# Performance work log

Hardware: AMD Instinct MI355X
Metric: run time of the kernel (lower is better)

Reference implementation:

```python
import jax, jax.numpy as jnp
import numpy as np

B, H, S, D = 8, 16, 1024, 64

def setup_inputs() -> dict:
    key = jax.random.key(0)
    kq, kk, kv, km = jax.random.split(key, 4)
    Q = jax.random.normal(kq, (B, H, S, D), dtype=jnp.float32)
    K = jax.random.normal(kk, (B, H, S, D), dtype=jnp.float32)
    V = jax.random.normal(kv, (B, H, S, D), dtype=jnp.float32)
    attn_mask = jax.random.randint(km, (B, H, S, S), 0, 2).astype(bool)
    return {"Q": Q, "K": K, "V": V, "attn_mask": attn_mask}

def reference(Q, K, V, attn_mask):
    # scores = Q @ K^T  (NOTE: source has no 1/sqrt(d) scaling)
    scores = jnp.einsum("bhqd,bhkd->bhqk", Q, K)
    # source uses masked_fill_(mask, 1e-9), i.e. masked positions become 1e-9 (not -inf)
    scores = jnp.where(attn_mask, jnp.float32(1e-9), scores)
    attn = jax.nn.softmax(scores, axis=-1)
    context = jnp.einsum("bhqk,bhkd->bhqd", attn, V)
    return context, attn
```

## Files before the change

### kernel.cpp

```cpp
#include <hip/hip_runtime.h>

#define Sn 1024
#define Dn 64
#define PH_LD 1032
#define K_LD 72
#define V_LD 72

typedef short v8s __attribute__((ext_vector_type(8)));
typedef unsigned short v8u __attribute__((ext_vector_type(8)));
typedef _Float16 v8h __attribute__((ext_vector_type(8)));
typedef float v4f __attribute__((ext_vector_type(4)));
typedef int   v4i __attribute__((ext_vector_type(4)));

#define LGKM0()  asm volatile("s_waitcnt lgkmcnt(0)" ::: "memory")
#define SBAR()   do { asm volatile("" ::: "memory"); __builtin_amdgcn_s_barrier(); \
                      __builtin_amdgcn_sched_barrier(0); } while (0)

__device__ __forceinline__ unsigned short f2bf(float x) {
    union { float f; unsigned u; } v; v.f = x;
    return (unsigned short)((v.u + 0x7FFFu + ((v.u >> 16) & 1u)) >> 16);
}
__device__ __forceinline__ float bf2f(unsigned short h) {
    union { float f; unsigned u; } v; v.u = ((unsigned)h) << 16;
    return v.f;
}
__device__ __forceinline__ void split2(float x, unsigned short& h, unsigned short& l) {
    unsigned short hs = f2bf(x);
    h = hs; l = f2bf(x - bf2f(hs));
}

__global__ __launch_bounds__(256) void prep_kh(const float* __restrict__ K,
    unsigned short* __restrict__ KF)
{
    const int bh = blockIdx.x >> 4, kt = blockIdx.x & 15;
    const int t = threadIdx.x;
    const int w = t >> 6, lane = t & 63;
    const int fr = lane & 15, g = lane >> 4;
    const float* src = K + (((size_t)(bh << 10) + (kt << 6) + (w << 4) + fr) << 6);
    const v4f a0 = __builtin_nontemporal_load((const v4f*)(src + (g << 3)));
    const v4f a1 = __builtin_nontemporal_load((const v4f*)(src + (g << 3) + 4));
    const v4f b0 = __builtin_nontemporal_load((const v4f*)(src + 32 + (g << 3)));
    const v4f b1 = __builtin_nontemporal_load((const v4f*)(src + 32 + (g << 3) + 4));
    v8h c0, c1;
    #pragma unroll
    for (int j = 0; j < 4; ++j) {
        c0[j] = (_Float16)a0[j]; c0[4 + j] = (_Float16)a1[j];
        c1[j] = (_Float16)b0[j]; c1[4 + j] = (_Float16)b1[j];
    }
    unsigned short* dst = KF + ((size_t)bh << 16) + ((size_t)((kt << 2) + w) << 10) + (lane << 3);
    *(v8h*)(dst)       = c0;
    *(v8h*)(dst + 512) = c1;
}

__global__ __launch_bounds__(256) void prep_vf(const float* __restrict__ V,
    unsigned short* __restrict__ VF)
{
    __shared__ float Ts[64][65];
    const int bh = blockIdx.x >> 4, kt = blockIdx.x & 15;
    const int t = threadIdx.x;
    {
        const int r = t >> 2, cs = (t & 3) << 4;
        const float* src = V + ((size_t)bh * Sn + (kt << 6) + r) * Dn + cs;
        const v4f a = __builtin_nontemporal_load((const v4f*)src);
        const v4f b = __builtin_nontemporal_load((const v4f*)src + 1);
        const v4f c = __builtin_nontemporal_load((const v4f*)src + 2);
        const v4f d = __builtin_nontemporal_load((const v4f*)src + 3);
        #pragma unroll
        for (int j = 0; j < 4; ++j) {
            Ts[r][cs + j]      = a[j];
            Ts[r][cs + 4 + j]  = b[j];
            Ts[r][cs + 8 + j]  = c[j];
            Ts[r][cs + 12 + j] = d[j];
        }
    }
    __syncthreads();
    {
        const int w = t >> 6, lane = t & 63;
        const int fr = lane & 15, g = lane >> 4;
        const int d = (w << 4) + fr;
        unsigned short* dst = VF + ((size_t)bh << 16) + ((size_t)((kt << 2) + w) << 10) + (lane << 3);
        v8u o0, o1;
        #pragma unroll
        for (int j = 0; j < 8; ++j) o0[j] = f2bf(Ts[(g << 3) + j][d]);
        #pragma unroll
        for (int j = 0; j < 8; ++j) o1[j] = f2bf(Ts[32 + (g << 3) + j][d]);
        *(v8u*)dst         = o0;
        *(v8u*)(dst + 512) = o1;
    }
}

__global__ __launch_bounds__(256) void prep_m(const int* __restrict__ M,
    unsigned long long* __restrict__ MW)
{
    const int NW = 2097152;
    const int lane = threadIdx.x & 63;
    const int wave = (blockIdx.x << 2) + (threadIdx.x >> 6);
    const int nwaves = gridDim.x << 2;
    for (int w0 = wave << 3; w0 < NW; w0 += nwaves << 3) {
        unsigned long long b[8];
        #pragma unroll
        for (int s = 0; s < 8; ++s) {
            const int v = __builtin_nontemporal_load(&M[((size_t)(w0 + s) << 6) + lane]);
            b[s] = __ballot(v != 0);
        }
        if (lane == 0) {
            ulonglong2* dst = (ulonglong2*)(MW + w0);
            ulonglong2 p0, p1, p2, p3;
            p0.x = b[0]; p0.y = b[1]; p1.x = b[2]; p1.y = b[3];
            p2.x = b[4]; p2.y = b[5]; p3.x = b[6]; p3.y = b[7];
            dst[0] = p0; dst[1] = p1; dst[2] = p2; dst[3] = p3;
        }
    }
}

__global__ __launch_bounds__(256, 4) void fused_attn_f(
    const unsigned short* __restrict__ KFG, const unsigned short* __restrict__ VFG,
    const float* __restrict__ Q, const unsigned long long* __restrict__ MW,
    float* __restrict__ attnO, float* __restrict__ ctxO)
{
    __shared__ unsigned short Ph[16][PH_LD];
    __shared__ float rsumW[4][16];
    __shared__ float invL[16];

    const int tid  = threadIdx.x;
    const int lane = tid & 63;
    const int w    = tid >> 6;
    const int fr   = lane & 15;
    const int g    = lane >> 4;

    const int swz = ((blockIdx.x & 7) << 10) + (blockIdx.x >> 3);
    const int bh = swz >> 6;
    const int q0 = (swz & 63) << 4;

    const float* Qb = Q + (size_t)bh * Sn * Dn + (size_t)q0 * Dn;
    float*       Ab = attnO + (size_t)bh * Sn * Sn + (size_t)q0 * Sn;
    float*       Cb = ctxO  + (size_t)bh * Sn * Dn + (size_t)q0 * Dn;
    const unsigned short* KFb = KFG + ((size_t)bh << 16);
    const unsigned short* VFb = VFG + ((size_t)bh << 16);
    const unsigned long long* mwp = MW + ((size_t)bh << 14) + ((size_t)(q0 + fr) << 4);

    v8h qf0, qf1;
    {
        const float* qp = Qb + fr * Dn + (g << 3);
        const v4f x0a = *(const v4f*)qp;
        const v4f x0b = *(const v4f*)(qp + 4);
        const v4f x1a = *(const v4f*)(qp + 32);
        const v4f x1b = *(const v4f*)(qp + 36);
        #pragma unroll
        for (int j = 0; j < 4; ++j) {
            qf0[j] = (_Float16)x0a[j]; qf0[4 + j] = (_Float16)x0b[j];
            qf1[j] = (_Float16)x1a[j]; qf1[4 + j] = (_Float16)x1b[j];
        }
    }

    const int sh = (w << 4) + (g << 2);

#define LDK(kt, k0_, k1_) do {                                                     \
        const unsigned short* _p = KFb + ((size_t)(((kt) << 2) + w) << 10) + (lane << 3); \
        k0_ = *(const v8h*)_p;  k1_ = *(const v8h*)(_p + 512);                     \
    } while (0)

#define STEPA(k0_, k1_, mwv, kt) do {                                              \
        v4f acc = {0.f, 0.f, 0.f, 0.f};                                            \
        __builtin_amdgcn_s_setprio(1);                                             \
        acc = __builtin_amdgcn_mfma_f32_16x16x32_f16(k0_, qf0, acc, 0, 0, 0);      \
        acc = __builtin_amdgcn_mfma_f32_16x16x32_f16(k1_, qf1, acc, 0, 0, 0);      \
        __builtin_amdgcn_s_setprio(0);                                             \
        const unsigned mb = (unsigned)((mwv) >> sh);                               \
        const float e0 = (mb & 1u) ? 1.0f : __expf(acc[0]);                        \
        const float e1 = (mb & 2u) ? 1.0f : __expf(acc[1]);                        \
        const float e2 = (mb & 4u) ? 1.0f : __expf(acc[2]);                        \
        const float e3 = (mb & 8u) ? 1.0f : __expf(acc[3]);                        \
        rs += (e0 + e1) + (e2 + e3);                                               \
        ushort4 pk;                                                                \
        pk.x = f2bf(e0); pk.y = f2bf(e1); pk.z = f2bf(e2); pk.w = f2bf(e3);        \
        *(ushort4*)&Ph[fr][((kt) << 6) + (w << 4) + (g << 2)] = pk;                \
    } while (0)

    float rs = 0.f;

    {
        v8h k0s[4], k1s[4];
        unsigned long long mk[4];
        LDK(0, k0s[0], k1s[0]);
        LDK(1, k0s[1], k1s[1]);
        LDK(2, k0s[2], k1s[2]);
        LDK(3, k0s[3], k1s[3]);
        mk[0] = mwp[0]; mk[1] = mwp[1]; mk[2] = mwp[2]; mk[3] = mwp[3];
        #pragma unroll
        for (int kt = 0; kt < 16; ++kt) {
            STEPA(k0s[kt & 3], k1s[kt & 3], mk[kt & 3], kt);
            if (kt + 4 < 16) {
                LDK(kt + 4, k0s[kt & 3], k1s[kt & 3]);
                mk[kt & 3] = mwp[kt + 4];
            }
        }
    }

    rs += __shfl_xor(rs, 16);
    rs += __shfl_xor(rs, 32);
    if (g == 0) rsumW[w][fr] = rs;
    __builtin_amdgcn_sched_barrier(0);
    LGKM0();
    SBAR();
    if (tid < 16) {
        const float s = rsumW[0][tid] + rsumW[1][tid] + rsumW[2][tid] + rsumW[3][tid];
        invL[tid] = 1.0f / s;
    }
    __builtin_amdgcn_sched_barrier(0);
    LGKM0();
    SBAR();

#define LDV(kt, v0_, v1_) do {                                                     \
        const unsigned short* _p = VFb + ((size_t)(((kt) << 2) + w) << 10) + (lane << 3); \
        v0_ = *(const v8s*)_p;  v1_ = *(const v8s*)(_p + 512);                     \
    } while (0)

#define STEPB(v0_, v1_, kt) do {                                                   \
        const v8s a0 = *(const v8s*)&Ph[fr][((kt) << 6) + (g << 3)];               \
        const v8s a1 = *(const v8s*)&Ph[fr][((kt) << 6) + 32 + (g << 3)];          \
        __builtin_amdgcn_s_setprio(1);                                             \
        accp = __builtin_amdgcn_mfma_f32_16x16x32_bf16(a0, v0_, accp, 0, 0, 0);    \
        accp = __builtin_amdgcn_mfma_f32_16x16x32_bf16(a1, v1_, accp, 0, 0, 0);    \
        __builtin_amdgcn_s_setprio(0);                                             \
    } while (0)

    v8s va0, va1, vb0, vb1;
    LDV(0, va0, va1);
    LDV(1, vb0, vb1);

    {
        const int qq = tid >> 4, ii = tid & 15;
        const float inv = invL[qq];
        float* arow = Ab + (size_t)qq * Sn;
        #pragma unroll
        for (int c = 0; c < 16; ++c) {
            const int k0 = (c << 6) + (ii << 2);
            const ushort4 p = *(const ushort4*)&Ph[qq][k0];
            v4f o;
            o[0] = bf2f(p.x) * inv; o[1] = bf2f(p.y) * inv;
            o[2] = bf2f(p.z) * inv; o[3] = bf2f(p.w) * inv;
            __builtin_nontemporal_store(o, (v4f*)(arow + k0));
        }
    }

    const int dcol = (w << 4) + fr;
    v4f accp = {0.f, 0.f, 0.f, 0.f};
    for (int kt = 0; kt < 16; kt += 2) {
        const int k2 = (kt + 2 < 16) ? kt + 2 : kt;
        const int k3 = (kt + 3 < 16) ? kt + 3 : kt;
        v8s vc0, vc1, vd0, vd1;
        LDV(k2, vc0, vc1);
        LDV(k3, vd0, vd1);
        STEPB(va0, va1, kt);
        STEPB(vb0, vb1, kt + 1);
        va0 = vc0; va1 = vc1;
        vb0 = vd0; vb1 = vd1;
    }
    #pragma unroll
    for (int r = 0; r < 4; ++r) {
        const int q = (g << 2) + r;
        __builtin_nontemporal_store(accp[r] * invL[q], &Cb[(size_t)q * Dn + dcol]);
    }
#undef LDK
#undef STEPA
#undef LDV
#undef STEPB
}

__global__ __launch_bounds__(256, 3) void fused_attn_fb(
    const float* __restrict__ Q, const float* __restrict__ K,
    const float* __restrict__ V, const int* __restrict__ M,
    float* __restrict__ attnO, float* __restrict__ ctxO)
{
    __shared__ unsigned short Ph[16][1048];
    __shared__ __align__(16) unsigned short Kraw[2 * 64 * K_LD];
    __shared__ float rsumW[4][16];
    __shared__ float invL[16];

    unsigned short (*Khi)[K_LD] = (unsigned short (*)[K_LD])Kraw;
    unsigned short (*Klo)[K_LD] = (unsigned short (*)[K_LD])(Kraw + 64 * K_LD);
    unsigned short (*Vt)[V_LD]  = (unsigned short (*)[V_LD])Kraw;

    const int tid  = threadIdx.x;
    const int lane = tid & 63;
    const int w    = tid >> 6;
    const int fr   = lane & 15;
    const int g    = lane >> 4;

    const int bh = blockIdx.x >> 6;
    const int q0 = (blockIdx.x & 63) << 4;

    const float* Qb = Q + (size_t)bh * Sn * Dn + (size_t)q0 * Dn;
    const float* Kb = K + (size_t)bh * Sn * Dn;
    const float* Vb = V + (size_t)bh * Sn * Dn;
    const int*   Mb = M + (size_t)bh * Sn * Sn + (size_t)q0 * Sn;
    float*       Ab = attnO + (size_t)bh * Sn * Sn + (size_t)q0 * Sn;
    float*       Cb = ctxO  + (size_t)bh * Sn * Dn + (size_t)q0 * Dn;

    v8s qh0, qh1, ql0, ql1;
    {
        const float* qp = Qb + fr * Dn + (g << 3);
        float x0[8], x1[8];
        *(v4f*)&x0[0] = *(const v4f*)qp;
        *(v4f*)&x0[4] = *(const v4f*)(qp + 4);
        *(v4f*)&x1[0] = *(const v4f*)(qp + 32);
        *(v4f*)&x1[4] = *(const v4f*)(qp + 36);
        #pragma unroll
        for (int i = 0; i < 8; ++i) {
            unsigned short hh, ll;
            split2(x0[i], hh, ll); qh0[i] = (short)hh; ql0[i] = (short)ll;
            split2(x1[i], hh, ll); qh1[i] = (short)hh; ql1[i] = (short)ll;
        }
    }

    const int srow = tid >> 4;
    const int sc4  = (tid & 15) << 2;

    const int* mp = Mb + (size_t)fr * Sn + (w << 4) + (g << 2);
    v4i mv = *(const v4i*)mp;

    v4f ka[4];
    #pragma unroll
    for (int i = 0; i < 4; ++i)
        ka[i] = *(const v4f*)(Kb + (size_t)(srow + (i << 4)) * Dn + sc4);

    float rs = 0.f;

    for (int kt = 0; kt < 16; ++kt) {
        __syncthreads();
        v4f kb[4];
        if (kt < 15) {
            const float* kn = Kb + (size_t)((kt + 1) << 6) * Dn;
            #pragma unroll
            for (int i = 0; i < 4; ++i)
                kb[i] = *(const v4f*)(kn + (size_t)(srow + (i << 4)) * Dn + sc4);
        }
        v4i mnext = mv;
        if (kt < 15) mnext = *(const v4i*)(mp + ((kt + 1) << 6));

        #pragma unroll
        for (int i = 0; i < 4; ++i) {
            const int row = srow + (i << 4);
            ushort4 hv, lv;
            split2(ka[i][0], hv.x, lv.x); split2(ka[i][1], hv.y, lv.y);
            split2(ka[i][2], hv.z, lv.z); split2(ka[i][3], hv.w, lv.w);
            *(ushort4*)&Khi[row][sc4] = hv;
            *(ushort4*)&Klo[row][sc4] = lv;
        }
        __syncthreads();

        const int krow = (w << 4) + fr;
        const v8s kh0 = *(const v8s*)&Khi[krow][(g << 3)];
        const v8s kh1 = *(const v8s*)&Khi[krow][32 + (g << 3)];
        const v8s kl0 = *(const v8s*)&Klo[krow][(g << 3)];
        const v8s kl1 = *(const v8s*)&Klo[krow][32 + (g << 3)];

        v4f acc = {0.f, 0.f, 0.f, 0.f};
        acc = __builtin_amdgcn_mfma_f32_16x16x32_bf16(kh0, qh0, acc, 0, 0, 0);
        acc = __builtin_amdgcn_mfma_f32_16x16x32_bf16(kh1, qh1, acc, 0, 0, 0);
        acc = __builtin_amdgcn_mfma_f32_16x16x32_bf16(kl0, qh0, acc, 0, 0, 0);
        acc = __builtin_amdgcn_mfma_f32_16x16x32_bf16(kl1, qh1, acc, 0, 0, 0);
        acc = __builtin_amdgcn_mfma_f32_16x16x32_bf16(kh0, ql0, acc, 0, 0, 0);
        acc = __builtin_amdgcn_mfma_f32_16x16x32_bf16(kh1, ql1, acc, 0, 0, 0);

        const float e0 = mv[0] ? 1.0f : __expf(acc[0]);
        const float e1 = mv[1] ? 1.0f : __expf(acc[1]);
        const float e2 = mv[2] ? 1.0f : __expf(acc[2]);
        const float e3 = mv[3] ? 1.0f : __expf(acc[3]);
        rs += (e0 + e1) + (e2 + e3);
        ushort4 pk;
        pk.x = f2bf(e0); pk.y = f2bf(e1); pk.z = f2bf(e2); pk.w = f2bf(e3);
        *(ushort4*)&Ph[fr][(kt << 6) + (w << 4) + (g << 2)] = pk;

        mv = mnext;
        #pragma unroll
        for (int i = 0; i < 4; ++i) ka[i] = kb[i];
    }

    rs += __shfl_xor(rs, 16);
    rs += __shfl_xor(rs, 32);
    if (g == 0) rsumW[w][fr] = rs;
    __syncthreads();
    if (tid < 16) {
        const float s = rsumW[0][tid] + rsumW[1][tid] + rsumW[2][tid] + rsumW[3][tid];
        invL[tid] = 1.0f / s;
    }
    __syncthreads();

    const int dcol = (w << 4) + fr;
    v4f va[4];
    #pragma unroll
    for (int i = 0; i < 4; ++i)
        va[i] = *(const v4f*)(Vb + (size_t)(srow + (i << 4)) * Dn + sc4);

    v4f accp = {0.f, 0.f, 0.f, 0.f};
    for (int kt = 0; kt < 16; ++kt) {
        __syncthreads();
        v4f vb[4];
        if (kt < 15) {
            const float* vn = Vb + (size_t)((kt + 1) << 6) * Dn;
            #pragma unroll
            for (int i = 0; i < 4; ++i)
                vb[i] = *(const v4f*)(vn + (size_t)(srow + (i << 4)) * Dn + sc4);
        }
        #pragma unroll
        for (int i = 0; i < 4; ++i) {
            const int row = srow + (i << 4);
            Vt[sc4 + 0][row] = f2bf(va[i][0]);
            Vt[sc4 + 1][row] = f2bf(va[i][1]);
            Vt[sc4 + 2][row] = f2bf(va[i][2]);
            Vt[sc4 + 3][row] = f2bf(va[i][3]);
        }
        __syncthreads();

        #pragma unroll
        for (int c = 0; c < 2; ++c) {
            const int kc = (kt << 6) + (c << 5);
            const v8s a = *(const v8s*)&Ph[fr][kc + (g << 3)];
            const v8s b = *(const v8s*)&Vt[dcol][(c << 5) + (g << 3)];
            accp = __builtin_amdgcn_mfma_f32_16x16x32_bf16(a, b, accp, 0, 0, 0);
        }
        #pragma unroll
        for (int i = 0; i < 4; ++i) va[i] = vb[i];
    }
    #pragma unroll
    for (int r = 0; r < 4; ++r) {
        const int q = (g << 2) + r;
        Cb[(size_t)q * Dn + dcol] = accp[r] * invL[q];
    }

    {
        const int qq = tid >> 4, ii = tid & 15;
        const float inv = invL[qq];
        float* arow = Ab + (size_t)qq * Sn;
        #pragma unroll
        for (int c = 0; c < 16; ++c) {
            const int k0 = (c << 6) + (ii << 2);
            const ushort4 p = *(const ushort4*)&Ph[qq][k0];
            v4f o;
            o[0] = bf2f(p.x) * inv; o[1] = bf2f(p.y) * inv;
            o[2] = bf2f(p.z) * inv; o[3] = bf2f(p.w) * inv;
            *(v4f*)(arow + k0) = o;
        }
    }
}

extern "C" void kernel_launch(void* const* d_in, const int* in_sizes, int n_in,
                              void* d_out, int out_size, void* d_ws, size_t ws_size,
                              hipStream_t stream) {
    const float* Q    = (const float*)d_in[0];
    const float* K    = (const float*)d_in[1];
    const float* V    = (const float*)d_in[2];
    const int*   mask = (const int*)d_in[3];

    float* ctx  = (float*)d_out;
    float* attn = (float*)d_out + (size_t)128 * Sn * Dn;

    const size_t NELEM = (size_t)128 * Sn * Dn;
    const size_t MWORDS = (size_t)128 * Sn * 16;
    const size_t NEED  = NELEM * 4 + MWORDS * 8;

    if (ws_size >= NEED) {
        unsigned short* KF = (unsigned short*)d_ws;
        unsigned short* VF = KF + NELEM;
        unsigned long long* MWp = (unsigned long long*)((char*)d_ws + NELEM * 4);
        prep_kh<<<2048, 256, 0, stream>>>(K, KF);
        prep_vf<<<2048, 256, 0, stream>>>(V, VF);
        prep_m<<<2048, 256, 0, stream>>>(mask, MWp);
        fused_attn_f<<<128 * 64, 256, 0, stream>>>(KF, VF, Q, MWp, attn, ctx);
    } else {
        fused_attn_fb<<<128 * 64, 256, 0, stream>>>(Q, K, V, mask, attn, ctx);
    }
}
```

Before: 263.5 us.

## Merge prep kernels into one launch and deepen V prefetch in PV loop

The three preprocessing kernels (K to fp16, V transpose to bf16, mask bit-packing) are merged into one launch that dispatches on block index, removing two launch boundaries and letting the three independent jobs run concurrently on the GPU. In the fused attention kernel, the PV loop is fully unrolled with a four-deep ring of V register buffers. The context store is moved ahead of the attention-probability write-out so the MFMA loop is no longer queued behind the large nontemporal attn stores. The merged kernel carries a 65-row shared tile even in branches that do not use it, which can limit occupancy for the K and mask blocks.

```diff
diff --git a/kernel.cpp b/kernel.cpp
--- a/kernel.cpp
+++ b/kernel.cpp
@@ -29,86 +29,85 @@
     h = hs; l = f2bf(x - bf2f(hs));
 }
 
-__global__ __launch_bounds__(256) void prep_kh(const float* __restrict__ K,
-    unsigned short* __restrict__ KF)
-{
-    const int bh = blockIdx.x >> 4, kt = blockIdx.x & 15;
-    const int t = threadIdx.x;
-    const int w = t >> 6, lane = t & 63;
-    const int fr = lane & 15, g = lane >> 4;
-    const float* src = K + (((size_t)(bh << 10) + (kt << 6) + (w << 4) + fr) << 6);
-    const v4f a0 = __builtin_nontemporal_load((const v4f*)(src + (g << 3)));
-    const v4f a1 = __builtin_nontemporal_load((const v4f*)(src + (g << 3) + 4));
-    const v4f b0 = __builtin_nontemporal_load((const v4f*)(src + 32 + (g << 3)));
-    const v4f b1 = __builtin_nontemporal_load((const v4f*)(src + 32 + (g << 3) + 4));
-    v8h c0, c1;
-    #pragma unroll
-    for (int j = 0; j < 4; ++j) {
-        c0[j] = (_Float16)a0[j]; c0[4 + j] = (_Float16)a1[j];
-        c1[j] = (_Float16)b0[j]; c1[4 + j] = (_Float16)b1[j];
-    }
-    unsigned short* dst = KF + ((size_t)bh << 16) + ((size_t)((kt << 2) + w) << 10) + (lane << 3);
-    *(v8h*)(dst)       = c0;
-    *(v8h*)(dst + 512) = c1;
-}
-
-__global__ __launch_bounds__(256) void prep_vf(const float* __restrict__ V,
-    unsigned short* __restrict__ VF)
+__global__ __launch_bounds__(256) void prep_all(
+    const float* __restrict__ K, const float* __restrict__ V,
+    const int* __restrict__ M,
+    unsigned short* __restrict__ KF, unsigned short* __restrict__ VF,
+    unsigned long long* __restrict__ MW)
 {
     __shared__ float Ts[64][65];
-    const int bh = blockIdx.x >> 4, kt = blockIdx.x & 15;
+    const int bid = blockIdx.x;
     const int t = threadIdx.x;
-    {
-        const int r = t >> 2, cs = (t & 3) << 4;
-        const float* src = V + ((size_t)bh * Sn + (kt << 6) + r) * Dn + cs;
-        const v4f a = __builtin_nontemporal_load((const v4f*)src);
-        const v4f b = __builtin_nontemporal_load((const v4f*)src + 1);
-        const v4f c = __builtin_nontemporal_load((const v4f*)src + 2);
-        const v4f d = __builtin_nontemporal_load((const v4f*)src + 3);
-        #pragma unroll
-        for (int j = 0; j < 4; ++j) {
-            Ts[r][cs + j]      = a[j];
-            Ts[r][cs + 4 + j]  = b[j];
-            Ts[r][cs + 8 + j]  = c[j];
-            Ts[r][cs + 12 + j] = d[j];
-        }
-    }
-    __syncthreads();
-    {
+
+    if (bid < 2048) {
+        const int bh = bid >> 4, kt = bid & 15;
         const int w = t >> 6, lane = t & 63;
         const int fr = lane & 15, g = lane >> 4;
-        const int d = (w << 4) + fr;
-        unsigned short* dst = VF + ((size_t)bh << 16) + ((size_t)((kt << 2) + w) << 10) + (lane << 3);
-        v8u o0, o1;
-        #pragma unroll
-        for (int j = 0; j < 8; ++j) o0[j] = f2bf(Ts[(g << 3) + j][d]);
-        #pragma unroll
-        for (int j = 0; j < 8; ++j) o1[j] = f2bf(Ts[32 + (g << 3) + j][d]);
-        *(v8u*)dst         = o0;
-        *(v8u*)(dst + 512) = o1;
-    }
-}
-
-__global__ __launch_bounds__(256) void prep_m(const int* __restrict__ M,
-    unsigned long long* __restrict__ MW)
-{
-    const int NW = 2097152;
-    const int lane = threadIdx.x & 63;
-    const int wave = (blockIdx.x << 2) + (threadIdx.x >> 6);
-    const int nwaves = gridDim.x << 2;
-    for (int w0 = wave << 3; w0 < NW; w0 += nwaves << 3) {
-        unsigned long long b[8];
-        #pragma unroll
-        for (int s = 0; s < 8; ++s) {
-            const int v = __builtin_nontemporal_load(&M[((size_t)(w0 + s) << 6) + lane]);
-            b[s] = __ballot(v != 0);
-        }
-        if (lane == 0) {
-            ulonglong2* dst = (ulonglong2*)(MW + w0);
-            ulonglong2 p0, p1, p2, p3;
-            p0.x = b[0]; p0.y = b[1]; p1.x = b[2]; p1.y = b[3];
-            p2.x = b[4]; p2.y = b[5]; p3.x = b[6]; p3.y = b[7];
-            dst[0] = p0; dst[1] = p1; dst[2] = p2; dst[3] = p3;
+        const float* src = K + (((size_t)(bh << 10) + (kt << 6) + (w << 4) + fr) << 6);
+        const v4f a0 = __builtin_nontemporal_load((const v4f*)(src + (g << 3)));
+        const v4f a1 = __builtin_nontemporal_load((const v4f*)(src + (g << 3) + 4));
+        const v4f b0 = __builtin_nontemporal_load((const v4f*)(src + 32 + (g << 3)));
+        const v4f b1 = __builtin_nontemporal_load((const v4f*)(src + 32 + (g << 3) + 4));
+        v8h c0, c1;
+        #pragma unroll
+        for (int j = 0; j < 4; ++j) {
+            c0[j] = (_Float16)a0[j]; c0[4 + j] = (_Float16)a1[j];
+            c1[j] = (_Float16)b0[j]; c1[4 + j] = (_Float16)b1[j];
+        }
+        unsigned short* dst = KF + ((size_t)bh << 16) + ((size_t)((kt << 2) + w) << 10) + (lane << 3);
+        *(v8h*)(dst)       = c0;
+        *(v8h*)(dst + 512) = c1;
+    } else if (bid < 4096) {
+        const int b2 = bid - 2048;
+        const int bh = b2 >> 4, kt = b2 & 15;
+        {
+            const int r = t >> 2, cs = (t & 3) << 4;
+            const float* src = V + ((size_t)bh * Sn + (kt << 6) + r) * Dn + cs;
+            const v4f a = __builtin_nontemporal_load((const v4f*)src);
+            const v4f b = __builtin_nontemporal_load((const v4f*)src + 1);
+            const v4f c = __builtin_nontemporal_load((const v4f*)src + 2);
+            const v4f d = __builtin_nontemporal_load((const v4f*)src + 3);
+            #pragma unroll
+            for (int j = 0; j < 4; ++j) {
+                Ts[r][cs + j]      = a[j];
+                Ts[r][cs + 4 + j]  = b[j];
+                Ts[r][cs + 8 + j]  = c[j];
+                Ts[r][cs + 12 + j] = d[j];
+            }
+        }
+        __syncthreads();
+        {
+            const int w = t >> 6, lane = t & 63;
+            const int fr = lane & 15, g = lane >> 4;
+            const int d = (w << 4) + fr;
+            unsigned short* dst = VF + ((size_t)bh << 16) + ((size_t)((kt << 2) + w) << 10) + (lane << 3);
+            v8u o0, o1;
+            #pragma unroll
+            for (int j = 0; j < 8; ++j) o0[j] = f2bf(Ts[(g << 3) + j][d]);
+            #pragma unroll
+            for (int j = 0; j < 8; ++j) o1[j] = f2bf(Ts[32 + (g << 3) + j][d]);
+            *(v8u*)dst         = o0;
+            *(v8u*)(dst + 512) = o1;
+        }
+    } else {
+        const int NW = 2097152;
+        const int lane = t & 63;
+        const int wave = ((bid - 4096) << 2) + (t >> 6);
+        const int nwaves = 2048 << 2;
+        for (int w0 = wave << 3; w0 < NW; w0 += nwaves << 3) {
+            unsigned long long b[8];
+            #pragma unroll
+            for (int s = 0; s < 8; ++s) {
+                const int v = __builtin_nontemporal_load(&M[((size_t)(w0 + s) << 6) + lane]);
+                b[s] = __ballot(v != 0);
+            }
+            if (lane == 0) {
+                ulonglong2* dst = (ulonglong2*)(MW + w0);
+                ulonglong2 p0, p1, p2, p3;
+                p0.x = b[0]; p0.y = b[1]; p1.x = b[2]; p1.y = b[3];
+                p2.x = b[4]; p2.y = b[5]; p3.x = b[6]; p3.y = b[7];
+                dst[0] = p0; dst[1] = p1; dst[2] = p2; dst[3] = p3;
+            }
         }
     }
 }
@@ -225,9 +224,25 @@
         __builtin_amdgcn_s_setprio(0);                                             \
     } while (0)
 
-    v8s va0, va1, vb0, vb1;
-    LDV(0, va0, va1);
-    LDV(1, vb0, vb1);
+    const int dcol = (w << 4) + fr;
+    v4f accp = {0.f, 0.f, 0.f, 0.f};
+    {
+        v8s v0s[4], v1s[4];
+        LDV(0, v0s[0], v1s[0]);
+        LDV(1, v0s[1], v1s[1]);
+        LDV(2, v0s[2], v1s[2]);
+        LDV(3, v0s[3], v1s[3]);
+        #pragma unroll
+        for (int kt = 0; kt < 16; ++kt) {
+            STEPB(v0s[kt & 3], v1s[kt & 3], kt);
+            if (kt + 4 < 16) LDV(kt + 4, v0s[kt & 3], v1s[kt & 3]);
+        }
+    }
+    #pragma unroll
+    for (int r = 0; r < 4; ++r) {
+        const int q = (g << 2) + r;
+        __builtin_nontemporal_store(accp[r] * invL[q], &Cb[(size_t)q * Dn + dcol]);
+    }
 
     {
         const int qq = tid >> 4, ii = tid & 15;
@@ -242,25 +257,6 @@
             o[2] = bf2f(p.z) * inv; o[3] = bf2f(p.w) * inv;
             __builtin_nontemporal_store(o, (v4f*)(arow + k0));
         }
-    }
-
-    const int dcol = (w << 4) + fr;
-    v4f accp = {0.f, 0.f, 0.f, 0.f};
-    for (int kt = 0; kt < 16; kt += 2) {
-        const int k2 = (kt + 2 < 16) ? kt + 2 : kt;
-        const int k3 = (kt + 3 < 16) ? kt + 3 : kt;
-        v8s vc0, vc1, vd0, vd1;
-        LDV(k2, vc0, vc1);
-        LDV(k3, vd0, vd1);
-        STEPB(va0, va1, kt);
-        STEPB(vb0, vb1, kt + 1);
-        va0 = vc0; va1 = vc1;
-        vb0 = vd0; vb1 = vd1;
-    }
-    #pragma unroll
-    for (int r = 0; r < 4; ++r) {
-        const int q = (g << 2) + r;
-        __builtin_nontemporal_store(accp[r] * invL[q], &Cb[(size_t)q * Dn + dcol]);
     }
 #undef LDK
 #undef STEPA
@@ -465,9 +461,7 @@
         unsigned short* KF = (unsigned short*)d_ws;
         unsigned short* VF = KF + NELEM;
         unsigned long long* MWp = (unsigned long long*)((char*)d_ws + NELEM * 4);
-        prep_kh<<<2048, 256, 0, stream>>>(K, KF);
-        prep_vf<<<2048, 256, 0, stream>>>(V, VF);
-        prep_m<<<2048, 256, 0, stream>>>(mask, MWp);
+        prep_all<<<6144, 256, 0, stream>>>(K, V, mask, KF, VF, MWp);
         fused_attn_f<<<128 * 64, 256, 0, stream>>>(KF, VF, Q, MWp, attn, ctx);
     } else {
         fused_attn_fb<<<128 * 64, 256, 0, stream>>>(Q, K, V, mask, attn, ctx);
```

Result: no change. 264.9 us (+0.5%).
